# Kernel tuning notes

Hardware: AMD Instinct MI355X
Metric: run time of the kernel (lower is better)

## Reference

```python
import jax, jax.numpy as jnp
import numpy as np

HID = 64   # hidden_dim
T = 256    # number of time points
B = 2048   # batch of initial conditions
DT = 0.05  # time step (t grid spacing)


def _xavier(k, shape, gain=0.5):
    fan_out, fan_in = shape
    std = gain * np.sqrt(2.0 / (fan_in + fan_out))
    return jax.random.normal(k, shape, dtype=jnp.float32) * std


def setup_inputs() -> dict:
    key = jax.random.key(0)
    ks = jax.random.split(key, 4)
    return {
        "t": jnp.arange(T, dtype=jnp.float32) * DT,
        "x0": jax.random.normal(ks[0], (B, 2), dtype=jnp.float32),
        "W1": _xavier(ks[1], (HID, 2)),
        "b1": jnp.zeros((HID,), jnp.float32),
        "W2": _xavier(ks[2], (HID, HID)),
        "b2": jnp.zeros((HID,), jnp.float32),
        "W3": _xavier(ks[3], (1, HID)),
        "b3": jnp.zeros((1,), jnp.float32),
    }


def reference(t, x0, W1, b1, W2, b2, W3, b3):
    """RK4 rollout of Hamiltonian dynamics. Returns trajectory [T, B, 2]."""

    def dynamics(x):
        h1 = jnp.tanh(x @ W1.T + b1)          # [B, H]
        h2 = jnp.tanh(h1 @ W2.T + b2)         # [B, H]
        # Analytic dH/dx via reverse chain (equivalent to autograd.grad):
        g2 = (1.0 - h2 * h2) * W3[0]          # [B, H]
        g1 = (1.0 - h1 * h1) * (g2 @ W2)      # [B, H]
        dHdx = g1 @ W1                        # [B, 2]  -> (dH/dq, dH/dp)
        # Hamilton's equations: dq/dt = dH/dp, dp/dt = -dH/dq
        return jnp.stack([dHdx[..., 1], -dHdx[..., 0]], axis=-1)

    dt = t[1] - t[0]

    def step(x, _):
        k1 = dynamics(x)
        k2 = dynamics(x + 0.5 * dt * k1)
        k3 = dynamics(x + 0.5 * dt * k2)
        k4 = dynamics(x + dt * k3)
        x_new = x + (dt / 6.0) * (k1 + 2.0 * k2 + 2.0 * k3 + k4)
        return x_new, x_new

    _, ys = jax.lax.scan(step, x0, None, length=t.shape[0] - 1)
    return jnp.concatenate([x0[None], ys], axis=0)  # [T, B, 2]
```

## Files before the change

kernel.cpp:

```cpp
#include <hip/hip_runtime.h>

#define HID    64
#define TSTEPS 256
#define BATCH  2048

typedef float v2f __attribute__((ext_vector_type(2)));

__device__ __forceinline__ float fast_tanh(float x) {
    float e = __builtin_amdgcn_exp2f(x * 2.8853900817779268f);
    float r = __builtin_amdgcn_rcpf(e + 1.0f);
    return fmaf(-2.0f, r, 1.0f);
}

template <int M>
__device__ __forceinline__ float swz(float v) {
    return __int_as_float(__builtin_amdgcn_ds_swizzle(
        __float_as_int(v), (M << 10) | 0x1F));
}

template <int CTRL>
__device__ __forceinline__ float dppx(float x) {
    int xi = __float_as_int(x);
    return __int_as_float(__builtin_amdgcn_update_dpp(xi, xi, CTRL, 0xF, 0xF, false));
}

__device__ __forceinline__ float bperm(int addr, float v) {
    return __int_as_float(__builtin_amdgcn_ds_bpermute(addr, __float_as_int(v)));
}

__device__ __forceinline__ void pkfma(v2f& acc, v2f w, v2f hv) {
    asm("v_pk_fma_f32 %0, %1, %2, %0" : "+v"(acc) : "v"(w), "v"(hv));
}

__device__ __forceinline__ float wave_sum(float v) {
    v += dppx<0x121>(v);
    v += dppx<0x122>(v);
    v += dppx<0x124>(v);
    v += dppx<0x128>(v);
    v += __int_as_float(__builtin_amdgcn_update_dpp(
            0, __float_as_int(v), 0x142, 0xA, 0xF, false));
    v += __int_as_float(__builtin_amdgcn_update_dpp(
            0, __float_as_int(v), 0x143, 0xC, 0xF, false));
    return __int_as_float(__builtin_amdgcn_readlane(__float_as_int(v), 63));
}

__device__ __forceinline__ int rev3(int x) {
    return ((x & 1) << 2) | (x & 2) | ((x >> 2) & 1);
}

__global__ __launch_bounds__(256) __attribute__((amdgpu_waves_per_eu(2, 2)))
void hnn_rk4_kernel(
        const float* __restrict__ tarr,
        const float* __restrict__ x0,
        const float* __restrict__ W1,
        const float* __restrict__ b1,
        const float* __restrict__ W2,
        const float* __restrict__ b2,
        const float* __restrict__ W3,
        float* __restrict__ out)
{
    const int lane = threadIdx.x & 63;
    const int wid  = threadIdx.x >> 6;
    const int b    = blockIdx.x * 4 + wid;

    const int rr = lane >> 3, cc = lane & 7;
    const int pc = rev3(cc),  pr = rev3(rr);
    const int uo = 8 * rr + pc;
    const int vu = 8 * cc + pr;

    const float dt  = tarr[1] - tarr[0];
    const float hdt = 0.5f * dt;
    const float sdt = dt * (1.0f / 6.0f);

    const float w1a = W1[2 * uo + 0];
    const float w1b = W1[2 * uo + 1];
    const float b1i = b1[uo];
    const float b2i = b2[uo];
    const float w3i = W3[uo];
    const float w1va = W1[2 * vu + 0];
    const float w1vb = W1[2 * vu + 1];

    int ba[8], br[8];
#pragma unroll
    for (int t = 0; t < 8; ++t) {
        ba[t] = (8 * cc + rev3(t)) * 4;
        br[t] = (8 * rr + rev3(t)) * 4;
    }
    int a32 = (lane ^ 32) * 4;
    int ath = (8 * cc + rr) * 4;

    v2f wsF[8][4], wsB[8][4];
#pragma unroll
    for (int t = 0; t < 8; ++t) {
#pragma unroll
        for (int m = 0; m < 4; ++m) {
            v2f f;
            f.x = W2[(8 * rr + ((2 * m)     ^ pc)) * HID + 8 * cc + t];
            f.y = W2[(8 * rr + ((2 * m + 1) ^ pc)) * HID + 8 * cc + t];
            wsF[t][m] = f;
            v2f g;
            g.x = W2[(8 * rr + t) * HID + 8 * cc + ((2 * m)     ^ pr)];
            g.y = W2[(8 * rr + t) * HID + 8 * cc + ((2 * m + 1) ^ pr)];
            wsB[t][m] = g;
        }
    }
#pragma unroll
    for (int t = 0; t < 8; ++t)
#pragma unroll
        for (int m = 0; m < 4; ++m)
            asm("" : "+v"(wsF[t][m]), "+v"(wsB[t][m]));

    float q = x0[2 * b + 0];
    float p = x0[2 * b + 1];

    if (lane == 0) {
        out[2 * b + 0] = q;
        out[2 * b + 1] = p;
    }

    auto dynamics = [&](float xq, float xp, float& kq, float& kp) {
        const float h1 = fast_tanh(fmaf(w1a, xq, fmaf(w1b, xp, b1i)));

        float hb[8];
#pragma unroll
        for (int t = 0; t < 8; ++t) hb[t] = bperm(ba[t], h1);
        const float h1v = bperm(ath, h1);

        v2f P0 = {0.f, 0.f}, P1 = {0.f, 0.f}, P2 = {0.f, 0.f}, P3 = {0.f, 0.f};
#pragma unroll
        for (int t = 0; t < 8; ++t) {
            v2f hv; hv.x = hb[t]; hv.y = hb[t];
            pkfma(P0, wsF[t][0], hv);
            pkfma(P1, wsF[t][1], hv);
            pkfma(P2, wsF[t][2], hv);
            pkfma(P3, wsF[t][3], hv);
        }
        P0.x += dppx<0xB1>(P2.x);  P0.y += dppx<0xB1>(P2.y);
        P1.x += dppx<0xB1>(P3.x);  P1.y += dppx<0xB1>(P3.y);
        P0.x += dppx<0x4E>(P1.x);  P0.y += dppx<0x4E>(P1.y);
        const float pre2 = P0.x + swz<4>(P0.y) + b2i;

        const float h2 = fast_tanh(pre2);
        const float g2 = w3i * fmaf(-h2, h2, 1.0f);

        float gb[8];
#pragma unroll
        for (int o = 0; o < 8; ++o) gb[o] = bperm(br[o], g2);

        v2f Q0 = {0.f, 0.f}, Q1 = {0.f, 0.f}, Q2 = {0.f, 0.f}, Q3 = {0.f, 0.f};
#pragma unroll
        for (int o = 0; o < 8; ++o) {
            v2f gv; gv.x = gb[o]; gv.y = gb[o];
            pkfma(Q0, wsB[o][0], gv);
            pkfma(Q1, wsB[o][1], gv);
            pkfma(Q2, wsB[o][2], gv);
            pkfma(Q3, wsB[o][3], gv);
        }
        Q0.x += dppx<0x128>(Q2.x);  Q0.y += dppx<0x128>(Q2.y);
        Q1.x += dppx<0x128>(Q3.x);  Q1.y += dppx<0x128>(Q3.y);
        Q0.x += swz<16>(Q1.x);      Q0.y += swz<16>(Q1.y);
        const float uv = Q0.x + bperm(a32, Q0.y);

        const float g1v = uv * fmaf(-h1v, h1v, 1.0f);

        kq =  wave_sum(g1v * w1vb);
        kp = -wave_sum(g1v * w1va);
    };

#pragma unroll 1
    for (int s = 0; s < TSTEPS - 1; ++s) {
        float kq1, kp1, kq2, kp2, kq3, kp3, kq4, kp4;
        dynamics(q, p, kq1, kp1);
        dynamics(fmaf(hdt, kq1, q), fmaf(hdt, kp1, p), kq2, kp2);
        dynamics(fmaf(hdt, kq2, q), fmaf(hdt, kp2, p), kq3, kp3);
        dynamics(fmaf(dt,  kq3, q), fmaf(dt,  kp3, p), kq4, kp4);
        q = fmaf(sdt, (kq1 + kq4) + 2.0f * (kq2 + kq3), q);
        p = fmaf(sdt, (kp1 + kp4) + 2.0f * (kp2 + kp3), p);
        if (lane == 0) {
            out[(s + 1) * (BATCH * 2) + 2 * b + 0] = q;
            out[(s + 1) * (BATCH * 2) + 2 * b + 1] = p;
        }
    }
}

extern "C" void kernel_launch(void* const* d_in, const int* in_sizes, int n_in,
                              void* d_out, int out_size, void* d_ws, size_t ws_size,
                              hipStream_t stream) {
    const float* t  = (const float*)d_in[0];
    const float* x0 = (const float*)d_in[1];
    const float* W1 = (const float*)d_in[2];
    const float* b1 = (const float*)d_in[3];
    const float* W2 = (const float*)d_in[4];
    const float* b2 = (const float*)d_in[5];
    const float* W3 = (const float*)d_in[6];

    hnn_rk4_kernel<<<dim3(BATCH / 4), dim3(256), 0, stream>>>(
        t, x0, W1, b1, W2, b2, W3, (float*)d_out);
}
```

Baseline: 750.0 us.

## Reuse forward W2 registers for backward pass and pack bpermuted operands

Drops the separate backward weight copy (wsB) and computes g2@W2 from the forward-layout registers, reducing a reduction-by-halving butterfly with conditional keep/send across lanes. Broadcast operands are packed into v2f pairs and fed via op_sel modifiers, removing the per-t duplication moves. This halves the W2 register footprint, which may reduce pressure and spills. The cost is extra select and cross-lane ops in the backward reduction.

```diff
diff --git a/kernel.cpp b/kernel.cpp
--- a/kernel.cpp
+++ b/kernel.cpp
@@ -30,6 +30,14 @@
 
 __device__ __forceinline__ void pkfma(v2f& acc, v2f w, v2f hv) {
     asm("v_pk_fma_f32 %0, %1, %2, %0" : "+v"(acc) : "v"(w), "v"(hv));
+}
+__device__ __forceinline__ void pkfma_lo(v2f& acc, v2f w, v2f h) {
+    asm("v_pk_fma_f32 %0, %1, %2, %0 op_sel_hi:[1,0,1]"
+        : "+v"(acc) : "v"(w), "v"(h));
+}
+__device__ __forceinline__ void pkfma_hi(v2f& acc, v2f w, v2f h) {
+    asm("v_pk_fma_f32 %0, %1, %2, %0 op_sel:[0,1,0] op_sel_hi:[1,1,1]"
+        : "+v"(acc) : "v"(w), "v"(h));
 }
 
 __device__ __forceinline__ float wave_sum(float v) {
@@ -44,7 +52,7 @@
     return __int_as_float(__builtin_amdgcn_readlane(__float_as_int(v), 63));
 }
 
-__device__ __forceinline__ int rev3(int x) {
+__device__ __forceinline__ constexpr int rev3(int x) {
     return ((x & 1) << 2) | (x & 2) | ((x >> 2) & 1);
 }
 
@@ -64,9 +72,9 @@
     const int b    = blockIdx.x * 4 + wid;
 
     const int rr = lane >> 3, cc = lane & 7;
-    const int pc = rev3(cc),  pr = rev3(rr);
+    const int pc = rev3(cc);
     const int uo = 8 * rr + pc;
-    const int vu = 8 * cc + pr;
+    const int vu = 8 * cc + rev3(rr);
 
     const float dt  = tarr[1] - tarr[0];
     const float hdt = 0.5f * dt;
@@ -80,16 +88,19 @@
     const float w1va = W1[2 * vu + 0];
     const float w1vb = W1[2 * vu + 1];
 
-    int ba[8], br[8];
-#pragma unroll
-    for (int t = 0; t < 8; ++t) {
-        ba[t] = (8 * cc + rev3(t)) * 4;
-        br[t] = (8 * rr + rev3(t)) * 4;
+    const int base_c = cc * 32;
+    const int base_r = rr * 32;
+    int ga[8];
+#pragma unroll
+    for (int m = 0; m < 4; ++m) {
+        const int e = rev3(2 * m);
+        ga[2 * m + 0] = base_r + ((e ^ cc) * 4);
+        ga[2 * m + 1] = base_r + (((e ^ 4) ^ cc) * 4);
     }
     int a32 = (lane ^ 32) * 4;
     int ath = (8 * cc + rr) * 4;
 
-    v2f wsF[8][4], wsB[8][4];
+    v2f wsF[8][4];
 #pragma unroll
     for (int t = 0; t < 8; ++t) {
 #pragma unroll
@@ -98,17 +109,15 @@
             f.x = W2[(8 * rr + ((2 * m)     ^ pc)) * HID + 8 * cc + t];
             f.y = W2[(8 * rr + ((2 * m + 1) ^ pc)) * HID + 8 * cc + t];
             wsF[t][m] = f;
-            v2f g;
-            g.x = W2[(8 * rr + t) * HID + 8 * cc + ((2 * m)     ^ pr)];
-            g.y = W2[(8 * rr + t) * HID + 8 * cc + ((2 * m + 1) ^ pr)];
-            wsB[t][m] = g;
         }
     }
 #pragma unroll
     for (int t = 0; t < 8; ++t)
 #pragma unroll
         for (int m = 0; m < 4; ++m)
-            asm("" : "+v"(wsF[t][m]), "+v"(wsB[t][m]));
+            asm("" : "+v"(wsF[t][m]));
+
+    const bool rb0 = lane & 8, rb1 = lane & 16, rb2 = lane & 32;
 
     float q = x0[2 * b + 0];
     float p = x0[2 * b + 1];
@@ -121,20 +130,31 @@
     auto dynamics = [&](float xq, float xp, float& kq, float& kp) {
         const float h1 = fast_tanh(fmaf(w1a, xq, fmaf(w1b, xp, b1i)));
 
-        float hb[8];
-#pragma unroll
-        for (int t = 0; t < 8; ++t) hb[t] = bperm(ba[t], h1);
+        v2f hp0, hp1, hp2, hp3;
+        hp0.x = bperm(base_c + 0 * 4, h1);  hp0.y = bperm(base_c + 4 * 4, h1);
+        hp1.x = bperm(base_c + 2 * 4, h1);  hp1.y = bperm(base_c + 6 * 4, h1);
+        hp2.x = bperm(base_c + 1 * 4, h1);  hp2.y = bperm(base_c + 5 * 4, h1);
+        hp3.x = bperm(base_c + 3 * 4, h1);  hp3.y = bperm(base_c + 7 * 4, h1);
         const float h1v = bperm(ath, h1);
 
         v2f P0 = {0.f, 0.f}, P1 = {0.f, 0.f}, P2 = {0.f, 0.f}, P3 = {0.f, 0.f};
-#pragma unroll
-        for (int t = 0; t < 8; ++t) {
-            v2f hv; hv.x = hb[t]; hv.y = hb[t];
-            pkfma(P0, wsF[t][0], hv);
-            pkfma(P1, wsF[t][1], hv);
-            pkfma(P2, wsF[t][2], hv);
-            pkfma(P3, wsF[t][3], hv);
-        }
+        pkfma_lo(P0, wsF[0][0], hp0); pkfma_lo(P1, wsF[0][1], hp0);
+        pkfma_lo(P2, wsF[0][2], hp0); pkfma_lo(P3, wsF[0][3], hp0);
+        pkfma_hi(P0, wsF[1][0], hp0); pkfma_hi(P1, wsF[1][1], hp0);
+        pkfma_hi(P2, wsF[1][2], hp0); pkfma_hi(P3, wsF[1][3], hp0);
+        pkfma_lo(P0, wsF[2][0], hp1); pkfma_lo(P1, wsF[2][1], hp1);
+        pkfma_lo(P2, wsF[2][2], hp1); pkfma_lo(P3, wsF[2][3], hp1);
+        pkfma_hi(P0, wsF[3][0], hp1); pkfma_hi(P1, wsF[3][1], hp1);
+        pkfma_hi(P2, wsF[3][2], hp1); pkfma_hi(P3, wsF[3][3], hp1);
+        pkfma_lo(P0, wsF[4][0], hp2); pkfma_lo(P1, wsF[4][1], hp2);
+        pkfma_lo(P2, wsF[4][2], hp2); pkfma_lo(P3, wsF[4][3], hp2);
+        pkfma_hi(P0, wsF[5][0], hp2); pkfma_hi(P1, wsF[5][1], hp2);
+        pkfma_hi(P2, wsF[5][2], hp2); pkfma_hi(P3, wsF[5][3], hp2);
+        pkfma_lo(P0, wsF[6][0], hp3); pkfma_lo(P1, wsF[6][1], hp3);
+        pkfma_lo(P2, wsF[6][2], hp3); pkfma_lo(P3, wsF[6][3], hp3);
+        pkfma_hi(P0, wsF[7][0], hp3); pkfma_hi(P1, wsF[7][1], hp3);
+        pkfma_hi(P2, wsF[7][2], hp3); pkfma_hi(P3, wsF[7][3], hp3);
+
         P0.x += dppx<0xB1>(P2.x);  P0.y += dppx<0xB1>(P2.y);
         P1.x += dppx<0xB1>(P3.x);  P1.y += dppx<0xB1>(P3.y);
         P0.x += dppx<0x4E>(P1.x);  P0.y += dppx<0x4E>(P1.y);
@@ -143,23 +163,40 @@
         const float h2 = fast_tanh(pre2);
         const float g2 = w3i * fmaf(-h2, h2, 1.0f);
 
-        float gb[8];
-#pragma unroll
-        for (int o = 0; o < 8; ++o) gb[o] = bperm(br[o], g2);
-
-        v2f Q0 = {0.f, 0.f}, Q1 = {0.f, 0.f}, Q2 = {0.f, 0.f}, Q3 = {0.f, 0.f};
-#pragma unroll
-        for (int o = 0; o < 8; ++o) {
-            v2f gv; gv.x = gb[o]; gv.y = gb[o];
-            pkfma(Q0, wsB[o][0], gv);
-            pkfma(Q1, wsB[o][1], gv);
-            pkfma(Q2, wsB[o][2], gv);
-            pkfma(Q3, wsB[o][3], gv);
-        }
-        Q0.x += dppx<0x128>(Q2.x);  Q0.y += dppx<0x128>(Q2.y);
-        Q1.x += dppx<0x128>(Q3.x);  Q1.y += dppx<0x128>(Q3.y);
-        Q0.x += swz<16>(Q1.x);      Q0.y += swz<16>(Q1.y);
-        const float uv = Q0.x + bperm(a32, Q0.y);
+        v2f gbp0, gbp1, gbp2, gbp3;
+        gbp0.x = bperm(ga[0], g2);  gbp0.y = bperm(ga[1], g2);
+        gbp1.x = bperm(ga[2], g2);  gbp1.y = bperm(ga[3], g2);
+        gbp2.x = bperm(ga[4], g2);  gbp2.y = bperm(ga[5], g2);
+        gbp3.x = bperm(ga[6], g2);  gbp3.y = bperm(ga[7], g2);
+
+        float uP[8];
+#pragma unroll
+        for (int t = 0; t < 8; ++t) {
+            v2f A = {0.f, 0.f};
+            pkfma(A, wsF[t][0], gbp0);
+            pkfma(A, wsF[t][1], gbp1);
+            pkfma(A, wsF[t][2], gbp2);
+            pkfma(A, wsF[t][3], gbp3);
+            uP[t] = A.x + A.y;
+        }
+
+        float v4[4];
+#pragma unroll
+        for (int t = 0; t < 4; ++t) {
+            float keep = rb0 ? uP[t + 4] : uP[t];
+            float send = rb0 ? uP[t]     : uP[t + 4];
+            v4[t] = keep + dppx<0x128>(send);
+        }
+        float w2v[2];
+#pragma unroll
+        for (int k = 0; k < 2; ++k) {
+            float keep = rb1 ? v4[k + 2] : v4[k];
+            float send = rb1 ? v4[k]     : v4[k + 2];
+            w2v[k] = keep + swz<16>(send);
+        }
+        float keep3 = rb2 ? w2v[1] : w2v[0];
+        float send3 = rb2 ? w2v[0] : w2v[1];
+        const float uv = keep3 + bperm(a32, send3);
 
         const float g1v = uv * fmaf(-h1v, h1v, 1.0f);
 
```

Measured after the change: 929.9 us. 1.24x slower.

## Process two batch trajectories per wavefront to interleave independent dependency chains

Applied to the files above, without the earlier changes.

Each wavefront now integrates two independent initial conditions (b and b+1024) at once, interleaving their MLP forward/backward passes so the latency of cross-lane permutes, DPP reductions and tanh can be hidden by the other chain's work. The grid is halved to 256 blocks and waves_per_eu is set to 1, which allows more registers per wave since the W2 tiles held in registers are now shared by both trajectories. Output stores become 8-byte vector writes. The trade-off is fewer waves in flight (256 blocks over 256 CUs, one wave per SIMD), so throughput depends entirely on instruction-level parallelism inside each wave.

```diff
diff --git a/kernel.cpp b/kernel.cpp
--- a/kernel.cpp
+++ b/kernel.cpp
@@ -44,11 +44,11 @@
     return __int_as_float(__builtin_amdgcn_readlane(__float_as_int(v), 63));
 }
 
-__device__ __forceinline__ int rev3(int x) {
+__device__ __forceinline__ constexpr int rev3(int x) {
     return ((x & 1) << 2) | (x & 2) | ((x >> 2) & 1);
 }
 
-__global__ __launch_bounds__(256) __attribute__((amdgpu_waves_per_eu(2, 2)))
+__global__ __launch_bounds__(256) __attribute__((amdgpu_waves_per_eu(1, 1)))
 void hnn_rk4_kernel(
         const float* __restrict__ tarr,
         const float* __restrict__ x0,
@@ -61,7 +61,9 @@
 {
     const int lane = threadIdx.x & 63;
     const int wid  = threadIdx.x >> 6;
-    const int b    = blockIdx.x * 4 + wid;
+    const int w    = blockIdx.x * 4 + wid;
+    const int bA   = w;
+    const int bB   = w + 1024;
 
     const int rr = lane >> 3, cc = lane & 7;
     const int pc = rev3(cc),  pr = rev3(rr);
@@ -110,75 +112,110 @@
         for (int m = 0; m < 4; ++m)
             asm("" : "+v"(wsF[t][m]), "+v"(wsB[t][m]));
 
-    float q = x0[2 * b + 0];
-    float p = x0[2 * b + 1];
-
+    float qA = x0[2 * bA + 0], pA = x0[2 * bA + 1];
+    float qB = x0[2 * bB + 0], pB = x0[2 * bB + 1];
+
+    v2f* out2 = (v2f*)out;
     if (lane == 0) {
-        out[2 * b + 0] = q;
-        out[2 * b + 1] = p;
-    }
-
-    auto dynamics = [&](float xq, float xp, float& kq, float& kp) {
-        const float h1 = fast_tanh(fmaf(w1a, xq, fmaf(w1b, xp, b1i)));
-
-        float hb[8];
-#pragma unroll
-        for (int t = 0; t < 8; ++t) hb[t] = bperm(ba[t], h1);
-        const float h1v = bperm(ath, h1);
-
-        v2f P0 = {0.f, 0.f}, P1 = {0.f, 0.f}, P2 = {0.f, 0.f}, P3 = {0.f, 0.f};
+        v2f oA; oA.x = qA; oA.y = pA;  out2[bA] = oA;
+        v2f oB; oB.x = qB; oB.y = pB;  out2[bB] = oB;
+    }
+
+    auto dyn2 = [&](float xqA, float xpA, float xqB, float xpB,
+                    float& kqA, float& kpA, float& kqB, float& kpB) {
+        const float h1A = fast_tanh(fmaf(w1a, xqA, fmaf(w1b, xpA, b1i)));
+        const float h1B = fast_tanh(fmaf(w1a, xqB, fmaf(w1b, xpB, b1i)));
+
+        float hbA[8], hbB[8];
 #pragma unroll
         for (int t = 0; t < 8; ++t) {
-            v2f hv; hv.x = hb[t]; hv.y = hb[t];
-            pkfma(P0, wsF[t][0], hv);
-            pkfma(P1, wsF[t][1], hv);
-            pkfma(P2, wsF[t][2], hv);
-            pkfma(P3, wsF[t][3], hv);
-        }
-        P0.x += dppx<0xB1>(P2.x);  P0.y += dppx<0xB1>(P2.y);
-        P1.x += dppx<0xB1>(P3.x);  P1.y += dppx<0xB1>(P3.y);
-        P0.x += dppx<0x4E>(P1.x);  P0.y += dppx<0x4E>(P1.y);
-        const float pre2 = P0.x + swz<4>(P0.y) + b2i;
-
-        const float h2 = fast_tanh(pre2);
-        const float g2 = w3i * fmaf(-h2, h2, 1.0f);
-
-        float gb[8];
-#pragma unroll
-        for (int o = 0; o < 8; ++o) gb[o] = bperm(br[o], g2);
-
-        v2f Q0 = {0.f, 0.f}, Q1 = {0.f, 0.f}, Q2 = {0.f, 0.f}, Q3 = {0.f, 0.f};
+            hbA[t] = bperm(ba[t], h1A);
+            hbB[t] = bperm(ba[t], h1B);
+        }
+        const float h1vA = bperm(ath, h1A);
+        const float h1vB = bperm(ath, h1B);
+
+        v2f PA0 = {0.f,0.f}, PA1 = {0.f,0.f}, PA2 = {0.f,0.f}, PA3 = {0.f,0.f};
+        v2f PB0 = {0.f,0.f}, PB1 = {0.f,0.f}, PB2 = {0.f,0.f}, PB3 = {0.f,0.f};
+#pragma unroll
+        for (int t = 0; t < 8; ++t) {
+            v2f hvA; hvA.x = hbA[t]; hvA.y = hbA[t];
+            v2f hvB; hvB.x = hbB[t]; hvB.y = hbB[t];
+            pkfma(PA0, wsF[t][0], hvA);  pkfma(PB0, wsF[t][0], hvB);
+            pkfma(PA1, wsF[t][1], hvA);  pkfma(PB1, wsF[t][1], hvB);
+            pkfma(PA2, wsF[t][2], hvA);  pkfma(PB2, wsF[t][2], hvB);
+            pkfma(PA3, wsF[t][3], hvA);  pkfma(PB3, wsF[t][3], hvB);
+        }
+        PA0.x += dppx<0xB1>(PA2.x);  PA0.y += dppx<0xB1>(PA2.y);
+        PB0.x += dppx<0xB1>(PB2.x);  PB0.y += dppx<0xB1>(PB2.y);
+        PA1.x += dppx<0xB1>(PA3.x);  PA1.y += dppx<0xB1>(PA3.y);
+        PB1.x += dppx<0xB1>(PB3.x);  PB1.y += dppx<0xB1>(PB3.y);
+        PA0.x += dppx<0x4E>(PA1.x);  PA0.y += dppx<0x4E>(PA1.y);
+        PB0.x += dppx<0x4E>(PB1.x);  PB0.y += dppx<0x4E>(PB1.y);
+        const float pre2A = PA0.x + swz<4>(PA0.y) + b2i;
+        const float pre2B = PB0.x + swz<4>(PB0.y) + b2i;
+
+        const float h2A = fast_tanh(pre2A);
+        const float h2B = fast_tanh(pre2B);
+        const float g2A = w3i * fmaf(-h2A, h2A, 1.0f);
+        const float g2B = w3i * fmaf(-h2B, h2B, 1.0f);
+
+        float gbA[8], gbB[8];
 #pragma unroll
         for (int o = 0; o < 8; ++o) {
-            v2f gv; gv.x = gb[o]; gv.y = gb[o];
-            pkfma(Q0, wsB[o][0], gv);
-            pkfma(Q1, wsB[o][1], gv);
-            pkfma(Q2, wsB[o][2], gv);
-            pkfma(Q3, wsB[o][3], gv);
-        }
-        Q0.x += dppx<0x128>(Q2.x);  Q0.y += dppx<0x128>(Q2.y);
-        Q1.x += dppx<0x128>(Q3.x);  Q1.y += dppx<0x128>(Q3.y);
-        Q0.x += swz<16>(Q1.x);      Q0.y += swz<16>(Q1.y);
-        const float uv = Q0.x + bperm(a32, Q0.y);
-
-        const float g1v = uv * fmaf(-h1v, h1v, 1.0f);
-
-        kq =  wave_sum(g1v * w1vb);
-        kp = -wave_sum(g1v * w1va);
+            gbA[o] = bperm(br[o], g2A);
+            gbB[o] = bperm(br[o], g2B);
+        }
+
+        v2f QA0 = {0.f,0.f}, QA1 = {0.f,0.f}, QA2 = {0.f,0.f}, QA3 = {0.f,0.f};
+        v2f QB0 = {0.f,0.f}, QB1 = {0.f,0.f}, QB2 = {0.f,0.f}, QB3 = {0.f,0.f};
+#pragma unroll
+        for (int o = 0; o < 8; ++o) {
+            v2f gvA; gvA.x = gbA[o]; gvA.y = gbA[o];
+            v2f gvB; gvB.x = gbB[o]; gvB.y = gbB[o];
+            pkfma(QA0, wsB[o][0], gvA);  pkfma(QB0, wsB[o][0], gvB);
+            pkfma(QA1, wsB[o][1], gvA);  pkfma(QB1, wsB[o][1], gvB);
+            pkfma(QA2, wsB[o][2], gvA);  pkfma(QB2, wsB[o][2], gvB);
+            pkfma(QA3, wsB[o][3], gvA);  pkfma(QB3, wsB[o][3], gvB);
+        }
+        QA0.x += dppx<0x128>(QA2.x);  QA0.y += dppx<0x128>(QA2.y);
+        QB0.x += dppx<0x128>(QB2.x);  QB0.y += dppx<0x128>(QB2.y);
+        QA1.x += dppx<0x128>(QA3.x);  QA1.y += dppx<0x128>(QA3.y);
+        QB1.x += dppx<0x128>(QB3.x);  QB1.y += dppx<0x128>(QB3.y);
+        QA0.x += swz<16>(QA1.x);      QA0.y += swz<16>(QA1.y);
+        QB0.x += swz<16>(QB1.x);      QB0.y += swz<16>(QB1.y);
+        const float uvA = QA0.x + bperm(a32, QA0.y);
+        const float uvB = QB0.x + bperm(a32, QB0.y);
+
+        const float g1vA = uvA * fmaf(-h1vA, h1vA, 1.0f);
+        const float g1vB = uvB * fmaf(-h1vB, h1vB, 1.0f);
+
+        kqA =  wave_sum(g1vA * w1vb);
+        kpA = -wave_sum(g1vA * w1va);
+        kqB =  wave_sum(g1vB * w1vb);
+        kpB = -wave_sum(g1vB * w1va);
     };
 
 #pragma unroll 1
     for (int s = 0; s < TSTEPS - 1; ++s) {
-        float kq1, kp1, kq2, kp2, kq3, kp3, kq4, kp4;
-        dynamics(q, p, kq1, kp1);
-        dynamics(fmaf(hdt, kq1, q), fmaf(hdt, kp1, p), kq2, kp2);
-        dynamics(fmaf(hdt, kq2, q), fmaf(hdt, kp2, p), kq3, kp3);
-        dynamics(fmaf(dt,  kq3, q), fmaf(dt,  kp3, p), kq4, kp4);
-        q = fmaf(sdt, (kq1 + kq4) + 2.0f * (kq2 + kq3), q);
-        p = fmaf(sdt, (kp1 + kp4) + 2.0f * (kp2 + kp3), p);
+        float kq1A,kp1A,kq2A,kp2A,kq3A,kp3A,kq4A,kp4A;
+        float kq1B,kp1B,kq2B,kp2B,kq3B,kp3B,kq4B,kp4B;
+        dyn2(qA, pA, qB, pB, kq1A, kp1A, kq1B, kp1B);
+        dyn2(fmaf(hdt, kq1A, qA), fmaf(hdt, kp1A, pA),
+             fmaf(hdt, kq1B, qB), fmaf(hdt, kp1B, pB), kq2A, kp2A, kq2B, kp2B);
+        dyn2(fmaf(hdt, kq2A, qA), fmaf(hdt, kp2A, pA),
+             fmaf(hdt, kq2B, qB), fmaf(hdt, kp2B, pB), kq3A, kp3A, kq3B, kp3B);
+        dyn2(fmaf(dt,  kq3A, qA), fmaf(dt,  kp3A, pA),
+             fmaf(dt,  kq3B, qB), fmaf(dt,  kp3B, pB), kq4A, kp4A, kq4B, kp4B);
+        qA = fmaf(sdt, (kq1A + kq4A) + 2.0f * (kq2A + kq3A), qA);
+        pA = fmaf(sdt, (kp1A + kp4A) + 2.0f * (kp2A + kp3A), pA);
+        qB = fmaf(sdt, (kq1B + kq4B) + 2.0f * (kq2B + kq3B), qB);
+        pB = fmaf(sdt, (kp1B + kp4B) + 2.0f * (kp2B + kp3B), pB);
         if (lane == 0) {
-            out[(s + 1) * (BATCH * 2) + 2 * b + 0] = q;
-            out[(s + 1) * (BATCH * 2) + 2 * b + 1] = p;
+            v2f oA; oA.x = qA; oA.y = pA;
+            v2f oB; oB.x = qB; oB.y = pB;
+            out2[(s + 1) * BATCH + bA] = oA;
+            out2[(s + 1) * BATCH + bB] = oB;
         }
     }
 }
@@ -194,6 +231,6 @@
     const float* b2 = (const float*)d_in[5];
     const float* W3 = (const float*)d_in[6];
 
-    hnn_rk4_kernel<<<dim3(BATCH / 4), dim3(256), 0, stream>>>(
+    hnn_rk4_kernel<<<dim3(BATCH / 8), dim3(256), 0, stream>>>(
         t, x0, W1, b1, W2, b2, W3, (float*)d_out);
 }
```

New measurement: 1.024 ms. 36.6% more time.
